# Performance work log

Measured on AMD Instinct MI355X. Metric: run time of the kernel, lower is better.

The kernel has to match this reference:

```python
import jax, jax.numpy as jnp
import numpy as np

N_CLS = 7  # only the first 7 channels contribute to the loss

def setup_inputs() -> dict:
    key = jax.random.key(0)
    k1, k2 = jax.random.split(key)
    pred = jax.random.normal(k1, (256, 16384, 8), dtype=jnp.float32)
    gt = jax.random.normal(k2, (256, 16384, 8), dtype=jnp.float32)
    return {"pred": pred, "gt": gt}

def reference(pred, gt):
    # per-batch loss: sum over objects and first 7 channels of squared error
    diff = pred[..., :N_CLS] - gt[..., :N_CLS]  # [B, N, 7]
    return jnp.sum(diff * diff, axis=(1, 2))    # [B]
```

## Files before the change

kernel.cpp:

```cpp
#include <hip/hip_runtime.h>


#define THREADS 256
#define SPLIT 8
#define F4_PER_BATCH (16384 * 2)
#define F4_PER_BLOCK (F4_PER_BATCH / SPLIT)
#define DEPTH 4
#define CHUNK (THREADS * DEPTH)
#define NCHUNK (F4_PER_BLOCK / CHUNK)

typedef float vfloat4 __attribute__((ext_vector_type(4)));

__global__ __launch_bounds__(THREADS) void label_loss_kernel(
    const vfloat4* __restrict__ pred,
    const vfloat4* __restrict__ gt,
    float* __restrict__ out)
{
    const int b   = blockIdx.x / SPLIT;
    const int seg = blockIdx.x % SPLIT;
    const long base = (long)b * F4_PER_BATCH + (long)seg * F4_PER_BLOCK
                    + threadIdx.x;

    const float m = (threadIdx.x & 1) ? 0.0f : 1.0f;

    vfloat4 Pa[DEPTH], Ga[DEPTH], Pb[DEPTH], Gb[DEPTH];
    float acc[DEPTH] = {0.0f, 0.0f, 0.0f, 0.0f};

#define LOAD(P_, G_, c) do {                                              \
    const long o_ = base + (long)(c) * CHUNK;                             \
    _Pragma("unroll")                                                     \
    for (int k = 0; k < DEPTH; ++k)                                       \
      P_[k] = __builtin_nontemporal_load(&pred[o_ + k * THREADS]);        \
    _Pragma("unroll")                                                     \
    for (int k = 0; k < DEPTH; ++k)                                       \
      G_[k] = __builtin_nontemporal_load(&gt[o_ + k * THREADS]);          \
  } while (0)

#define CONSUME(P_, G_) do {                                              \
    _Pragma("unroll")                                                     \
    for (int k = 0; k < DEPTH; ++k) {                                     \
      const vfloat4 d_ = P_[k] - G_[k];                                   \
      acc[k] += d_.x * d_.x + d_.y * d_.y + d_.z * d_.z + m * (d_.w * d_.w); \
    }                                                                     \
  } while (0)

    LOAD(Pa, Ga, 0);

    #pragma unroll 1
    for (int c = 0; c + 2 < NCHUNK; c += 2) {
        LOAD(Pb, Gb, c + 1);
        CONSUME(Pa, Ga);
        LOAD(Pa, Ga, c + 2);
        CONSUME(Pb, Gb);
    }
    LOAD(Pb, Gb, NCHUNK - 1);
    CONSUME(Pa, Ga);
    CONSUME(Pb, Gb);

#undef LOAD
#undef CONSUME

    float v = (acc[0] + acc[1]) + (acc[2] + acc[3]);

    #pragma unroll
    for (int off = 32; off > 0; off >>= 1)
        v += __shfl_down(v, off, 64);

    __shared__ float wsum[THREADS / 64];
    const int lane = threadIdx.x & 63;
    const int wave = threadIdx.x >> 6;
    if (lane == 0) wsum[wave] = v;
    __syncthreads();

    if (threadIdx.x == 0) {
        atomicAdd(&out[b], wsum[0] + wsum[1] + wsum[2] + wsum[3]);
    }
}

extern "C" void kernel_launch(void* const* d_in, const int* in_sizes, int n_in,
                              void* d_out, int out_size, void* d_ws, size_t ws_size,
                              hipStream_t stream) {
    const vfloat4* pred = (const vfloat4*)d_in[0];
    const vfloat4* gt   = (const vfloat4*)d_in[1];
    float* out = (float*)d_out;

    (void)hipMemsetAsync(d_out, 0, (size_t)out_size * sizeof(float), stream);

    const int n_blocks = 256 * SPLIT;
    label_loss_kernel<<<dim3(n_blocks), dim3(THREADS), 0, stream>>>(pred, gt, out);
}
```

Before: 249.0 us.

## Stream inputs directly into LDS with double-buffered global_load_lds

Register-staged nontemporal vector loads are replaced with `global_load_lds` transfers that write 16-byte elements straight into a double-buffered shared-memory area. Explicit `vmcnt` waits overlap the next stage's fetch with consuming the current one. The aim is to cut VGPR pressure and issue overhead on a purely bandwidth-bound reduction. In exchange, each thread now has only two loads in flight per stage instead of eight, which reduces memory-level parallelism.

```diff
diff --git a/kernel.cpp b/kernel.cpp
--- a/kernel.cpp
+++ b/kernel.cpp
@@ -5,9 +5,7 @@
 #define SPLIT 8
 #define F4_PER_BATCH (16384 * 2)
 #define F4_PER_BLOCK (F4_PER_BATCH / SPLIT)
-#define DEPTH 4
-#define CHUNK (THREADS * DEPTH)
-#define NCHUNK (F4_PER_BLOCK / CHUNK)
+#define NCHUNK (F4_PER_BLOCK / THREADS)
 
 typedef float vfloat4 __attribute__((ext_vector_type(4)));
 
@@ -16,63 +14,69 @@
     const vfloat4* __restrict__ gt,
     float* __restrict__ out)
 {
-    const int b   = blockIdx.x / SPLIT;
-    const int seg = blockIdx.x % SPLIT;
-    const long base = (long)b * F4_PER_BATCH + (long)seg * F4_PER_BLOCK
-                    + threadIdx.x;
+    __shared__ vfloat4 lbuf[2][2][THREADS];
 
-    const float m = (threadIdx.x & 1) ? 0.0f : 1.0f;
+    const int tid  = (int)threadIdx.x;
+    const int wave = tid >> 6;
+    const int b    = blockIdx.x / SPLIT;
+    const int seg  = blockIdx.x % SPLIT;
+    const int base_f4 = b * F4_PER_BATCH + seg * F4_PER_BLOCK + tid;
 
-    vfloat4 Pa[DEPTH], Ga[DEPTH], Pb[DEPTH], Gb[DEPTH];
-    float acc[DEPTH] = {0.0f, 0.0f, 0.0f, 0.0f};
+    const float m = (tid & 1) ? 0.0f : 1.0f;
 
-#define LOAD(P_, G_, c) do {                                              \
-    const long o_ = base + (long)(c) * CHUNK;                             \
-    _Pragma("unroll")                                                     \
-    for (int k = 0; k < DEPTH; ++k)                                       \
-      P_[k] = __builtin_nontemporal_load(&pred[o_ + k * THREADS]);        \
-    _Pragma("unroll")                                                     \
-    for (int k = 0; k < DEPTH; ++k)                                       \
-      G_[k] = __builtin_nontemporal_load(&gt[o_ + k * THREADS]);          \
+#define GLD_LDS(gp_, lp_)                                                   \
+    __builtin_amdgcn_global_load_lds(                                       \
+        (const __attribute__((address_space(1))) unsigned*)(gp_),           \
+        (__attribute__((address_space(3))) unsigned*)(lp_), 16, 0, 2)
+
+#define STAGE(s_, c_) do {                                                  \
+    const int g_ = base_f4 + (c_) * THREADS;                                \
+    GLD_LDS(&pred[g_], &lbuf[s_][0][wave << 6]);                            \
+    GLD_LDS(&gt[g_],   &lbuf[s_][1][wave << 6]);                            \
   } while (0)
 
-#define CONSUME(P_, G_) do {                                              \
-    _Pragma("unroll")                                                     \
-    for (int k = 0; k < DEPTH; ++k) {                                     \
-      const vfloat4 d_ = P_[k] - G_[k];                                   \
-      acc[k] += d_.x * d_.x + d_.y * d_.y + d_.z * d_.z + m * (d_.w * d_.w); \
-    }                                                                     \
+#define WAITN(n_) do {                                                      \
+    asm volatile("s_waitcnt vmcnt(" #n_ ")" ::: "memory");                  \
+    __builtin_amdgcn_sched_barrier(0);                                      \
   } while (0)
 
-    LOAD(Pa, Ga, 0);
+    float acc = 0.0f;
 
-    #pragma unroll 1
-    for (int c = 0; c + 2 < NCHUNK; c += 2) {
-        LOAD(Pb, Gb, c + 1);
-        CONSUME(Pa, Ga);
-        LOAD(Pa, Ga, c + 2);
-        CONSUME(Pb, Gb);
+#define CONSUME(s_) do {                                                    \
+    const vfloat4 P_ = lbuf[s_][0][tid];                                    \
+    const vfloat4 G_ = lbuf[s_][1][tid];                                    \
+    const vfloat4 d_ = P_ - G_;                                             \
+    acc += d_.x * d_.x + d_.y * d_.y + d_.z * d_.z + m * (d_.w * d_.w);     \
+  } while (0)
+
+    STAGE(0, 0);
+
+    #pragma unroll
+    for (int c = 0; c < NCHUNK - 1; ++c) {
+        STAGE((c + 1) & 1, c + 1);
+        WAITN(2);
+        CONSUME(c & 1);
     }
-    LOAD(Pb, Gb, NCHUNK - 1);
-    CONSUME(Pa, Ga);
-    CONSUME(Pb, Gb);
+    WAITN(0);
+    CONSUME((NCHUNK - 1) & 1);
 
-#undef LOAD
+#undef STAGE
+#undef WAITN
 #undef CONSUME
+#undef GLD_LDS
 
-    float v = (acc[0] + acc[1]) + (acc[2] + acc[3]);
+    float v = acc;
 
     #pragma unroll
     for (int off = 32; off > 0; off >>= 1)
         v += __shfl_down(v, off, 64);
 
     __shared__ float wsum[THREADS / 64];
-    const int lane = threadIdx.x & 63;
-    const int wave = threadIdx.x >> 6;
+    const int lane = tid & 63;
     if (lane == 0) wsum[wave] = v;
     __syncthreads();
 
-    if (threadIdx.x == 0) {
+    if (tid == 0) {
         atomicAdd(&out[b], wsum[0] + wsum[1] + wsum[2] + wsum[3]);
     }
 }
```

New measurement: 249.6 us. No clear change (+0.3%).

## Use one 1024-thread block per batch and drop memset and atomics

Applied to the files above, without the earlier changes.

Each batch row is now reduced by a single 1024-thread block instead of eight 256-thread blocks. The block writes its final sum directly, so the output memset and the atomicAdd are no longer needed, and one launch is removed. The cost is a grid of only 256 blocks, roughly one per CU, which may leave less memory parallelism in flight to saturate HBM bandwidth.

```diff
diff --git a/kernel.cpp b/kernel.cpp
--- a/kernel.cpp
+++ b/kernel.cpp
@@ -1,13 +1,11 @@
 #include <hip/hip_runtime.h>
 
 
-#define THREADS 256
-#define SPLIT 8
+#define THREADS 1024
 #define F4_PER_BATCH (16384 * 2)
-#define F4_PER_BLOCK (F4_PER_BATCH / SPLIT)
 #define DEPTH 4
 #define CHUNK (THREADS * DEPTH)
-#define NCHUNK (F4_PER_BLOCK / CHUNK)
+#define NCHUNK (F4_PER_BATCH / CHUNK)
 
 typedef float vfloat4 __attribute__((ext_vector_type(4)));
 
@@ -16,18 +14,17 @@
     const vfloat4* __restrict__ gt,
     float* __restrict__ out)
 {
-    const int b   = blockIdx.x / SPLIT;
-    const int seg = blockIdx.x % SPLIT;
-    const long base = (long)b * F4_PER_BATCH + (long)seg * F4_PER_BLOCK
-                    + threadIdx.x;
+    const int tid = (int)threadIdx.x;
+    const int b   = blockIdx.x;
+    const int base_f4 = b * F4_PER_BATCH + tid;
 
-    const float m = (threadIdx.x & 1) ? 0.0f : 1.0f;
+    const float m = (tid & 1) ? 0.0f : 1.0f;
 
     vfloat4 Pa[DEPTH], Ga[DEPTH], Pb[DEPTH], Gb[DEPTH];
     float acc[DEPTH] = {0.0f, 0.0f, 0.0f, 0.0f};
 
 #define LOAD(P_, G_, c) do {                                              \
-    const long o_ = base + (long)(c) * CHUNK;                             \
+    const int o_ = base_f4 + (c) * CHUNK;                                 \
     _Pragma("unroll")                                                     \
     for (int k = 0; k < DEPTH; ++k)                                       \
       P_[k] = __builtin_nontemporal_load(&pred[o_ + k * THREADS]);        \
@@ -67,13 +64,16 @@
         v += __shfl_down(v, off, 64);
 
     __shared__ float wsum[THREADS / 64];
-    const int lane = threadIdx.x & 63;
-    const int wave = threadIdx.x >> 6;
+    const int lane = tid & 63;
+    const int wave = tid >> 6;
     if (lane == 0) wsum[wave] = v;
     __syncthreads();
 
-    if (threadIdx.x == 0) {
-        atomicAdd(&out[b], wsum[0] + wsum[1] + wsum[2] + wsum[3]);
+    if (tid == 0) {
+        float s = 0.0f;
+        #pragma unroll
+        for (int w = 0; w < THREADS / 64; ++w) s += wsum[w];
+        out[b] = s;
     }
 }
 
@@ -84,8 +84,5 @@
     const vfloat4* gt   = (const vfloat4*)d_in[1];
     float* out = (float*)d_out;
 
-    (void)hipMemsetAsync(d_out, 0, (size_t)out_size * sizeof(float), stream);
-
-    const int n_blocks = 256 * SPLIT;
-    label_loss_kernel<<<dim3(n_blocks), dim3(THREADS), 0, stream>>>(pred, gt, out);
+    label_loss_kernel<<<dim3(256), dim3(THREADS), 0, stream>>>(pred, gt, out);
 }
```

After: 254.3 us. +2.1%, slower.
